# Performance work log

Hardware: AMD Instinct MI355X
Metric: run time of the kernel (lower is better)

Reference implementation:

```python
import jax, jax.numpy as jnp
import numpy as np
import math

B, N, D, H = 2, 2048, 512, 8
DH = D // H
HID = int(D * 16 / 3)  # 2730, SwiGLU hidden; chunks into 1365+1365
EPS = 1e-5


def _get_slopes(n):
    # n=8 is a power of two
    start = 2.0 ** (-2.0 ** (-(math.log2(n) - 3)))
    return np.array([start * (start ** i) for i in range(n)], dtype=np.float32)

_SLOPES = jnp.asarray(_get_slopes(H))  # [H]


def _ln(x, w, b):
    m = jnp.mean(x, axis=-1, keepdims=True)
    v = jnp.mean((x - m) ** 2, axis=-1, keepdims=True)
    return (x - m) * jax.lax.rsqrt(v + EPS) * w + b


def setup_inputs() -> dict:
    key = jax.random.key(0)
    ks = jax.random.split(key, 20)
    p = lambda k, s: jax.random.normal(k, s, jnp.float32) * 0.02
    return {
        "x": jax.random.normal(ks[0], (B, N, D), jnp.float32),
        "coords": jax.random.uniform(ks[1], (B, N, 2), jnp.float32) * 100.0,
        "q_w": p(ks[2], (D, D)), "q_b": jnp.zeros((D,), jnp.float32),
        "k_w": p(ks[3], (D, D)), "k_b": jnp.zeros((D,), jnp.float32),
        "v_w": p(ks[4], (D, D)), "v_b": jnp.zeros((D,), jnp.float32),
        "o_w": p(ks[5], (D, D)), "o_b": jnp.zeros((D,), jnp.float32),
        "gamma1": jnp.ones((D,), jnp.float32),
        "ln1_w": jnp.ones((D,), jnp.float32), "ln1_b": jnp.zeros((D,), jnp.float32),
        "fc1_w": p(ks[6], (HID, D)), "fc1_b": jnp.zeros((HID,), jnp.float32),
        "fc2_w": p(ks[7], (D, HID // 2)), "fc2_b": jnp.zeros((D,), jnp.float32),
        "gamma2": jnp.ones((D,), jnp.float32),
        "ln2_w": jnp.ones((D,), jnp.float32), "ln2_b": jnp.zeros((D,), jnp.float32),
    }


def reference(x, coords, q_w, q_b, k_w, k_b, v_w, v_b, o_w, o_b, gamma1,
              ln1_w, ln1_b, fc1_w, fc1_b, fc2_w, fc2_b, gamma2, ln2_w, ln2_b):
    # ---- residual1: distance-ALiBi attention (eval mode: x + gamma1*attn(norm(x)))
    xn = _ln(x, ln1_w, ln1_b)
    q = (xn @ q_w.T + q_b).reshape(B, N, H, DH).transpose(0, 2, 1, 3)  # [b,h,n,dh]
    k = (xn @ k_w.T + k_b).reshape(B, N, H, DH).transpose(0, 2, 1, 3)
    v = (xn @ v_w.T + v_b).reshape(B, N, H, DH).transpose(0, 2, 1, 3)
    # pairwise Euclidean distance of tile coords -> [b,n,n]
    diff = coords[:, :, None, :] - coords[:, None, :, :]
    dist = jnp.sqrt(jnp.sum(diff * diff, axis=-1))
    attn_bias = -_SLOPES[None, :, None, None] * dist[:, None, :, :]  # [b,h,n,n]
    scale = 1.0 / math.sqrt(DH)
    scores = jnp.einsum('bhqd,bhkd->bhqk', q, k) * scale + attn_bias
    attn = jax.nn.softmax(scores, axis=-1)
    ctx = jnp.einsum('bhqk,bhkd->bhqd', attn, v)
    ctx = ctx.transpose(0, 2, 1, 3).reshape(B, N, D)
    attn_out = ctx @ o_w.T + o_b
    x = x + gamma1 * attn_out
    # ---- residual2: SwiGLU-style MLP (eval mode: x + gamma2*mlp(norm(x)))
    xn2 = _ln(x, ln2_w, ln2_b)
    hpre = xn2 @ fc1_w.T + fc1_b  # [b,n,HID]
    h1, h2 = jnp.split(hpre, 2, axis=-1)
    mlp_out = (jax.nn.silu(h1) * h2) @ fc2_w.T + fc2_b
    return x + gamma2 * mlp_out
```

## Files before the change

### kernel.cpp

```cpp
#include <hip/hip_runtime.h>
#include <math.h>

#define Bdim  2
#define Nseq  2048
#define Dmod  512
#define Hn    8
#define DHd   64
#define HID   2730
#define HHALF 1365
#define HC    1408
#define NPACK 2816
#define ROWS  4096
#define NSPLIT 2
#define KT_PER (Nseq / 64 / NSPLIT)

typedef __bf16 bf16x8 __attribute__((ext_vector_type(8)));
typedef __bf16 bf16x4 __attribute__((ext_vector_type(4)));
typedef float  f32x4  __attribute__((ext_vector_type(4)));

__device__ __forceinline__ void glds16(const __bf16* g, __bf16* l) {
    __builtin_amdgcn_global_load_lds(
        (const __attribute__((address_space(1))) void*)g,
        (__attribute__((address_space(3))) void*)l, 16, 0, 0);
}

__device__ __forceinline__ void ln_body(
    int row, int tid, const float* __restrict__ x, const float* __restrict__ w,
    const float* __restrict__ b, __bf16* __restrict__ out)
{
    const float* xr = x + (size_t)row * Dmod;
    float2 v = *(const float2*)(xr + tid * 2);
    float s  = v.x + v.y;
    float sq = v.x * v.x + v.y * v.y;
#pragma unroll
    for (int m = 1; m < 64; m <<= 1) {
        s  += __shfl_xor(s, m, 64);
        sq += __shfl_xor(sq, m, 64);
    }
    __shared__ float ss[4], ssq[4];
    const int wv = tid >> 6;
    if ((tid & 63) == 0) { ss[wv] = s; ssq[wv] = sq; }
    __syncthreads();
    s  = ss[0] + ss[1] + ss[2] + ss[3];
    sq = ssq[0] + ssq[1] + ssq[2] + ssq[3];
    const float mean = s * (1.0f / Dmod);
    const float var  = sq * (1.0f / Dmod) - mean * mean;
    const float rstd = rsqrtf(var + 1e-5f);
    float2 wv2 = *(const float2*)(w + tid * 2);
    float2 bv2 = *(const float2*)(b + tid * 2);
    __bf16* orow = out + (size_t)row * Dmod + tid * 2;
    orow[0] = (__bf16)((v.x - mean) * rstd * wv2.x + bv2.x);
    orow[1] = (__bf16)((v.y - mean) * rstd * wv2.y + bv2.y);
}

#define SEG0 (1536*512)
#define SEG1 (512*512)
#define SEG2 (NPACK*512)
#define SEG3 (512*HC)
#define CONV_BLOCKS ((SEG0 + SEG1 + SEG2 + SEG3) / 256)
__global__ __launch_bounds__(256) void convert_ln(
    const float* __restrict__ q_w, const float* __restrict__ k_w,
    const float* __restrict__ v_w, const float* __restrict__ o_w,
    const float* __restrict__ fc1_w, const float* __restrict__ fc2_w,
    __bf16* __restrict__ wqkv, __bf16* __restrict__ wo,
    __bf16* __restrict__ wfc1p, __bf16* __restrict__ wfc2p,
    const float* __restrict__ x, const float* __restrict__ ln1w,
    const float* __restrict__ ln1b, __bf16* __restrict__ xn)
{
    if (blockIdx.x >= CONV_BLOCKS) {
        ln_body(blockIdx.x - CONV_BLOCKS, threadIdx.x, x, ln1w, ln1b, xn);
        return;
    }
    int idx = blockIdx.x * 256 + threadIdx.x;
    if (idx < SEG0) {
        int n = idx >> 9, k = idx & 511;
        float v = (n < 512) ? q_w[n * 512 + k]
                : (n < 1024) ? k_w[(n - 512) * 512 + k]
                : v_w[(n - 1024) * 512 + k];
        wqkv[idx] = (__bf16)v;
        return;
    }
    idx -= SEG0;
    if (idx < SEG1) { wo[idx] = (__bf16)o_w[idx]; return; }
    idx -= SEG1;
    if (idx < SEG2) {
        int n = idx >> 9, k = idx & 511;
        int j = n >> 5, u = n & 31;
        int base = j * 16 + (u & 15);
        float v = 0.0f;
        if (base < HHALF) {
            int hidx = base + ((u & 16) ? HHALF : 0);
            v = fc1_w[(size_t)hidx * 512 + k];
        }
        wfc1p[idx] = (__bf16)v;
        return;
    }
    idx -= SEG2;
    if (idx < SEG3) {
        int n = idx / HC, k = idx - n * HC;
        float v = (k < HHALF) ? fc2_w[(size_t)n * HHALF + k] : 0.0f;
        wfc2p[idx] = (__bf16)v;
    }
}

__global__ __launch_bounds__(256) void ln_kernel(
    const float* __restrict__ x, const float* __restrict__ w,
    const float* __restrict__ b, __bf16* __restrict__ out)
{
    ln_body(blockIdx.x, threadIdx.x, x, w, b, out);
}

__global__ __launch_bounds__(512) void gemm_res(
    const __bf16* __restrict__ A, int lda,
    const __bf16* __restrict__ Bw, int ldb,
    const float* __restrict__ bias, int K,
    float* __restrict__ out_f32, int ld_out,
    const float* __restrict__ res, const float* __restrict__ g)
{
    __shared__ __bf16 smem[2 * 64 * 64];
    __bf16* As = smem;
    __bf16* Bs = smem + 64 * 64;
    const int tid  = threadIdx.x;
    const int wave = tid >> 6, lane = tid & 63;
    const int t    = lane & 15, quad = lane >> 4;
    const int kg   = wave >> 2, wv = wave & 3;
    const int m0   = blockIdx.x * 64;
    const int n0   = blockIdx.y * 64;

    const int srow = tid >> 3;
    const int gch  = ((tid & 7) ^ (srow & 7)) * 8;
    const __bf16* aptr = A  + (size_t)(m0 + srow) * lda + gch;
    const __bf16* bptr = Bw + (size_t)(n0 + srow) * ldb + gch;

    const int arow = wv * 16 + t;
    const int aoff = arow * 64 + (((kg * 4 + quad) ^ (arow & 7)) * 8);
    int boffs[4];
#pragma unroll
    for (int ct = 0; ct < 4; ++ct) {
        int brow = ct * 16 + t;
        boffs[ct] = brow * 64 + (((kg * 4 + quad) ^ (brow & 7)) * 8);
    }

    f32x4 acc[4] = {};
    for (int k0 = 0; k0 < K; k0 += 64) {
        __syncthreads();
        glds16(aptr + k0, As + tid * 8);
        glds16(bptr + k0, Bs + tid * 8);
        __syncthreads();
        bf16x8 a = *(const bf16x8*)(As + aoff);
#pragma unroll
        for (int ct = 0; ct < 4; ++ct) {
            bf16x8 b = *(const bf16x8*)(Bs + boffs[ct]);
            acc[ct] = __builtin_amdgcn_mfma_f32_16x16x32_bf16(a, b, acc[ct], 0, 0, 0);
        }
    }

    __syncthreads();
    if (kg == 1) {
        float* dst = (float*)smem + ((size_t)wv * 64 + lane) * 16;
#pragma unroll
        for (int ct = 0; ct < 4; ++ct) *(f32x4*)(dst + ct * 4) = acc[ct];
    }
    __syncthreads();
    if (kg == 0) {
        const float* src = (const float*)smem + ((size_t)wv * 64 + lane) * 16;
        const int row_base = m0 + wv * 16 + quad * 4;
#pragma unroll
        for (int ct = 0; ct < 4; ++ct) {
            f32x4 other = *(const f32x4*)(src + ct * 4);
            const int col = n0 + ct * 16 + t;
            const float bb = bias[col];
#pragma unroll
            for (int r = 0; r < 4; ++r) {
                const int row = row_base + r;
                out_f32[(size_t)row * ld_out + col] =
                    res[(size_t)row * ld_out + col] +
                    g[col] * (acc[ct][r] + other[r] + bb);
            }
        }
    }
}

#define LDT 136
__global__ __launch_bounds__(256) void qkv_gemm128(
    const __bf16* __restrict__ A, const __bf16* __restrict__ W,
    const float* __restrict__ qb_, const float* __restrict__ kb_,
    const float* __restrict__ vb_,
    __bf16* __restrict__ qk, __bf16* __restrict__ vtg)
{
    __shared__ __bf16 smem[64 * LDT];
    __bf16* As = smem;
    __bf16* Bs = smem + 4096;
    const int tid  = threadIdx.x;
    const int wave = tid >> 6, lane = tid & 63;
    const int t    = lane & 15, quad = lane >> 4;
    const int m0   = blockIdx.x * 128, n0 = blockIdx.y * 128;
    const int mr   = (wave & 1) * 64,  nr = (wave >> 1) * 64;
    const int ra0 = tid >> 2,          ca0 = (tid & 3) * 8;
    const int ra1 = (tid + 256) >> 2,  ca1 = (tid & 3) * 8;

    f32x4 acc[4][4] = {};

    for (int k0 = 0; k0 < Dmod; k0 += 32) {
        __syncthreads();
        glds16(A + (size_t)(m0 + ra0) * Dmod + k0 + ca0, As + tid * 8);
        glds16(A + (size_t)(m0 + ra1) * Dmod + k0 + ca1, As + (tid + 256) * 8);
        glds16(W + (size_t)(n0 + ra0) * Dmod + k0 + ca0, Bs + tid * 8);
        glds16(W + (size_t)(n0 + ra1) * Dmod + k0 + ca1, Bs + (tid + 256) * 8);
        __syncthreads();
        bf16x8 af[4], bfr[4];
#pragma unroll
        for (int mi = 0; mi < 4; ++mi)
            af[mi] = *(const bf16x8*)(As + (mr + mi * 16 + t) * 32 + quad * 8);
#pragma unroll
        for (int ni = 0; ni < 4; ++ni)
            bfr[ni] = *(const bf16x8*)(Bs + (nr + ni * 16 + t) * 32 + quad * 8);
#pragma unroll
        for (int mi = 0; mi < 4; ++mi)
#pragma unroll
            for (int ni = 0; ni < 4; ++ni)
                acc[mi][ni] = __builtin_amdgcn_mfma_f32_16x16x32_bf16(af[mi], bfr[ni], acc[mi][ni], 0, 0, 0);
    }

    const int y = blockIdx.y;
    if (y < 8) {
#pragma unroll
        for (int mi = 0; mi < 4; ++mi) {
            const int row_base = m0 + mr + mi * 16 + quad * 4;
#pragma unroll
            for (int ni = 0; ni < 4; ++ni) {
                const int col = n0 + nr + ni * 16 + t;
                const float bb = (col < 512) ? qb_[col] : kb_[col - 512];
#pragma unroll
                for (int r = 0; r < 4; ++r)
                    qk[(size_t)(row_base + r) * 1024 + col] = (__bf16)(acc[mi][ni][r] + bb);
            }
        }
    } else {
        const int tok0 = m0 & 2047;
        const int bI   = m0 >> 11;
#pragma unroll
        for (int half = 0; half < 2; ++half) {
            __syncthreads();
            if ((wave >> 1) == half) {
#pragma unroll
                for (int ni = 0; ni < 4; ++ni) {
                    const int dh = ni * 16 + t;
                    const float bb = vb_[(y - 8) * 128 + half * 64 + dh];
#pragma unroll
                    for (int mi = 0; mi < 4; ++mi) {
                        const int n = mr + mi * 16 + quad * 4;
                        bf16x4 pk;
#pragma unroll
                        for (int r = 0; r < 4; ++r) pk[r] = (__bf16)(acc[mi][ni][r] + bb);
                        *(bf16x4*)(smem + dh * LDT + n) = pk;
                    }
                }
            }
            __syncthreads();
            const int hh = (y - 8) * 2 + half;
            const size_t rowbase = (size_t)(bI * 8 + hh) * 64;
#pragma unroll
            for (int j = 0; j < 4; ++j) {
                int chunk = tid + j * 256;
                int dr = chunk >> 4, cc = (chunk & 15) * 8;
                bf16x8 vv = *(const bf16x8*)(smem + dr * LDT + cc);
                *(bf16x8*)(vtg + (rowbase + dr) * Nseq + tok0 + cc) = vv;
            }
        }
    }
}

__global__ __launch_bounds__(256) void fc1_gemm128(
    const __bf16* __restrict__ A, const __bf16* __restrict__ W,
    const float* __restrict__ fc1_b_, __bf16* __restrict__ out)
{
    __shared__ __bf16 As[128 * 32];
    __shared__ __bf16 Bs[128 * 32];
    const int tid  = threadIdx.x;
    const int wave = tid >> 6, lane = tid & 63;
    const int t    = lane & 15, quad = lane >> 4;
    const int m0   = blockIdx.x * 128, n0 = blockIdx.y * 128;
    const int mr   = (wave & 1) * 64,  nr = (wave >> 1) * 64;
    const int ra0 = tid >> 2,          ca0 = (tid & 3) * 8;
    const int ra1 = (tid + 256) >> 2,  ca1 = (tid & 3) * 8;

    f32x4 acc[4][4] = {};

    for (int k0 = 0; k0 < Dmod; k0 += 32) {
        __syncthreads();
        glds16(A + (size_t)(m0 + ra0) * Dmod + k0 + ca0, As + tid * 8);
        glds16(A + (size_t)(m0 + ra1) * Dmod + k0 + ca1, As + (tid + 256) * 8);
        glds16(W + (size_t)(n0 + ra0) * Dmod + k0 + ca0, Bs + tid * 8);
        glds16(W + (size_t)(n0 + ra1) * Dmod + k0 + ca1, Bs + (tid + 256) * 8);
        __syncthreads();
        bf16x8 af[4], bfr[4];
#pragma unroll
        for (int mi = 0; mi < 4; ++mi)
            af[mi] = *(const bf16x8*)(As + (mr + mi * 16 + t) * 32 + quad * 8);
#pragma unroll
        for (int ni = 0; ni < 4; ++ni)
            bfr[ni] = *(const bf16x8*)(Bs + (nr + ni * 16 + t) * 32 + quad * 8);
#pragma unroll
        for (int mi = 0; mi < 4; ++mi)
#pragma unroll
            for (int ni = 0; ni < 4; ++ni)
                acc[mi][ni] = __builtin_amdgcn_mfma_f32_16x16x32_bf16(af[mi], bfr[ni], acc[mi][ni], 0, 0, 0);
    }

#pragma unroll
    for (int mi = 0; mi < 4; ++mi) {
        const int row_base = m0 + mr + mi * 16 + quad * 4;
#pragma unroll
        for (int gI = 0; gI < 2; ++gI) {
            const int base = n0 + nr + gI * 32;
            const int hb = (base >> 5) * 16 + t;
            const bool valid = hb < HHALF;
            const float b1 = valid ? fc1_b_[hb] : 0.0f;
            const float b2 = valid ? fc1_b_[HHALF + hb] : 0.0f;
#pragma unroll
            for (int r = 0; r < 4; ++r) {
                float a = acc[mi][2 * gI][r] + b1;
                float c = acc[mi][2 * gI + 1][r] + b2;
                float sw = a / (1.0f + __expf(-a)) * c;
                out[(size_t)(row_base + r) * HC + hb] = (__bf16)sw;
            }
        }
    }
}

__global__ __launch_bounds__(256) void attn_kernel(
    const __bf16* __restrict__ qk, const __bf16* __restrict__ vt,
    const float* __restrict__ coords,
    __bf16* __restrict__ op, float* __restrict__ lp)
{
    constexpr int LD = 72;
    __shared__ __bf16 Ks[64][LD];
    __shared__ __bf16 Vt[64][LD];
    __shared__ __bf16 Ps[64][LD];
    __shared__ float2 kco[64];

    const int qt = blockIdx.x, h = blockIdx.y;
    const int s = blockIdx.z >> 1, b = blockIdx.z & 1;
    const int bh = b * Hn + h;
    const int tid = threadIdx.x;
    const int wave = tid >> 6, lane = tid & 63;
    const int t = lane & 15, quad = lane >> 4;
    const float c1 = 0.125f * 1.44269504f;
    const float d1 = exp2f(-(float)(h + 1)) * 1.44269504f;
    const int kt0 = s * KT_PER, kt1 = kt0 + KT_PER;

    const int qrow = qt * 64 + wave * 16 + t;
    const size_t qbase = (size_t)(b * Nseq + qrow) * 1024 + h * DHd;
    bf16x8 bq0 = *(const bf16x8*)(qk + qbase + quad * 8);
    bf16x8 bq1 = *(const bf16x8*)(qk + qbase + 32 + quad * 8);
    float2 qc = *(const float2*)(coords + (size_t)(b * Nseq + qrow) * 2);
    const float qx = qc.x, qy = qc.y;

    const int sr = tid >> 3, scc = (tid & 7) * 8;
    const __bf16* kbase = qk + (size_t)(b * Nseq) * 1024 + 512 + h * DHd;
    const __bf16* vbase = vt + (size_t)(bh * 64) * Nseq;

    bf16x8 kreg0, kreg1, vreg0, vreg1;
    float2 kcreg = {0.f, 0.f};
    {
        const int kn0 = kt0 * 64;
        kreg0 = *(const bf16x8*)(kbase + (size_t)(kn0 + sr) * 1024 + scc);
        kreg1 = *(const bf16x8*)(kbase + (size_t)(kn0 + sr + 32) * 1024 + scc);
        vreg0 = *(const bf16x8*)(vbase + (size_t)sr * Nseq + kn0 + scc);
        vreg1 = *(const bf16x8*)(vbase + (size_t)(sr + 32) * Nseq + kn0 + scc);
        if (tid < 64) kcreg = *(const float2*)(coords + (size_t)(b * Nseq + kn0 + tid) * 2);
    }

    f32x4 o[4] = {};
    float lrun = 0.0f;

    for (int kt = kt0; kt < kt1; ++kt) {
        __syncthreads();
        *(bf16x8*)(&Ks[sr][scc])      = kreg0;
        *(bf16x8*)(&Ks[sr + 32][scc]) = kreg1;
        *(bf16x8*)(&Vt[sr][scc])      = vreg0;
        *(bf16x8*)(&Vt[sr + 32][scc]) = vreg1;
        if (tid < 64) kco[tid] = kcreg;
        __syncthreads();
        if (kt + 1 < kt1) {
            const int kn = (kt + 1) * 64;
            kreg0 = *(const bf16x8*)(kbase + (size_t)(kn + sr) * 1024 + scc);
            kreg1 = *(const bf16x8*)(kbase + (size_t)(kn + sr + 32) * 1024 + scc);
            vreg0 = *(const bf16x8*)(vbase + (size_t)sr * Nseq + kn + scc);
            vreg1 = *(const bf16x8*)(vbase + (size_t)(sr + 32) * Nseq + kn + scc);
            if (tid < 64) kcreg = *(const float2*)(coords + (size_t)(b * Nseq + kn + tid) * 2);
        }

        f32x4 sA[4];
#pragma unroll
        for (int am = 0; am < 4; ++am) {
            bf16x8 a0 = *(const bf16x8*)(&Ks[am * 16 + t][quad * 8]);
            bf16x8 a1 = *(const bf16x8*)(&Ks[am * 16 + t][32 + quad * 8]);
            f32x4 z = {};
            z = __builtin_amdgcn_mfma_f32_16x16x32_bf16(a0, bq0, z, 0, 0, 0);
            sA[am] = __builtin_amdgcn_mfma_f32_16x16x32_bf16(a1, bq1, z, 0, 0, 0);
        }

        float p[4][4];
#pragma unroll
        for (int am = 0; am < 4; ++am)
#pragma unroll
            for (int r = 0; r < 4; ++r) {
                float2 kc = kco[am * 16 + quad * 4 + r];
                float dx = qx - kc.x, dy = qy - kc.y;
                float dist = __builtin_amdgcn_sqrtf(dx * dx + dy * dy);
                float e = __builtin_amdgcn_exp2f(sA[am][r] * c1 - d1 * dist);
                p[am][r] = e;
                lrun += e;
            }

#pragma unroll
        for (int am = 0; am < 4; ++am) {
            bf16x4 pk;
#pragma unroll
            for (int r = 0; r < 4; ++r) pk[r] = (__bf16)p[am][r];
            *(bf16x4*)(&Ps[wave * 16 + t][am * 16 + quad * 4]) = pk;
        }

        bf16x8 ap0 = *(const bf16x8*)(&Ps[wave * 16 + t][quad * 8]);
        bf16x8 ap1 = *(const bf16x8*)(&Ps[wave * 16 + t][32 + quad * 8]);
#pragma unroll
        for (int ct = 0; ct < 4; ++ct) {
            bf16x8 bv0 = *(const bf16x8*)(&Vt[ct * 16 + t][quad * 8]);
            bf16x8 bv1 = *(const bf16x8*)(&Vt[ct * 16 + t][32 + quad * 8]);
            o[ct] = __builtin_amdgcn_mfma_f32_16x16x32_bf16(ap0, bv0, o[ct], 0, 0, 0);
            o[ct] = __builtin_amdgcn_mfma_f32_16x16x32_bf16(ap1, bv1, o[ct], 0, 0, 0);
        }
    }

    lrun += __shfl_xor(lrun, 16, 64);
    lrun += __shfl_xor(lrun, 32, 64);
    if (quad == 0)
        lp[(((size_t)s * Bdim + b) * Hn + h) * Nseq + qt * 64 + wave * 16 + t] = lrun;

    const int orow_base = qt * 64 + wave * 16 + quad * 4;
#pragma unroll
    for (int ct = 0; ct < 4; ++ct)
#pragma unroll
        for (int r = 0; r < 4; ++r) {
            size_t row = (size_t)s * ROWS + b * Nseq + orow_base + r;
            op[row * Dmod + h * DHd + ct * 16 + t] = (__bf16)o[ct][r];
        }
}

__global__ __launch_bounds__(256) void merge_kernel(
    const __bf16* __restrict__ op, const float* __restrict__ lp,
    __bf16* __restrict__ ctx)
{
    int idx = blockIdx.x * 256 + threadIdx.x;
    int row = idx >> 7, c4 = (idx & 127) * 4;
    int h = c4 >> 6;
    int b = row >> 11, n = row & 2047;
    float l = 0.0f;
#pragma unroll
    for (int s = 0; s < NSPLIT; ++s)
        l += lp[(((size_t)s * Bdim + b) * Hn + h) * Nseq + n];
    float rl = __builtin_amdgcn_rcpf(l);
    float oa[4] = {0.f, 0.f, 0.f, 0.f};
#pragma unroll
    for (int s = 0; s < NSPLIT; ++s) {
        bf16x4 ov = *(const bf16x4*)(op + ((size_t)s * ROWS + row) * Dmod + c4);
#pragma unroll
        for (int j = 0; j < 4; ++j) oa[j] += (float)ov[j];
    }
    bf16x4 r;
#pragma unroll
    for (int j = 0; j < 4; ++j) r[j] = (__bf16)(oa[j] * rl);
    *(bf16x4*)(ctx + (size_t)row * Dmod + c4) = r;
}

extern "C" void kernel_launch(void* const* d_in, const int* in_sizes, int n_in,
                              void* d_out, int out_size, void* d_ws, size_t ws_size,
                              hipStream_t stream)
{
    (void)in_sizes; (void)n_in; (void)out_size; (void)ws_size;
    const float* x      = (const float*)d_in[0];
    const float* coords = (const float*)d_in[1];
    const float* q_w    = (const float*)d_in[2];
    const float* q_b    = (const float*)d_in[3];
    const float* k_w    = (const float*)d_in[4];
    const float* k_b    = (const float*)d_in[5];
    const float* v_w    = (const float*)d_in[6];
    const float* v_b    = (const float*)d_in[7];
    const float* o_w    = (const float*)d_in[8];
    const float* o_b    = (const float*)d_in[9];
    const float* gamma1 = (const float*)d_in[10];
    const float* ln1_w  = (const float*)d_in[11];
    const float* ln1_b  = (const float*)d_in[12];
    const float* fc1_w  = (const float*)d_in[13];
    const float* fc1_b  = (const float*)d_in[14];
    const float* fc2_w  = (const float*)d_in[15];
    const float* fc2_b  = (const float*)d_in[16];
    const float* gamma2 = (const float*)d_in[17];
    const float* ln2_w  = (const float*)d_in[18];
    const float* ln2_b  = (const float*)d_in[19];

    size_t off = 0;
    auto alloc = [&](size_t bytes) {
        void* p = (char*)d_ws + off;
        off += (bytes + 255) & ~(size_t)255;
        return p;
    };
    __bf16* wqkv  = (__bf16*)alloc((size_t)1536 * 512 * 2);
    __bf16* wo    = (__bf16*)alloc((size_t)512 * 512 * 2);
    __bf16* wfc1p = (__bf16*)alloc((size_t)NPACK * 512 * 2);
    __bf16* wfc2p = (__bf16*)alloc((size_t)512 * HC * 2);
    __bf16* xn    = (__bf16*)alloc((size_t)ROWS * Dmod * 2);
    __bf16* xn2   = (__bf16*)alloc((size_t)ROWS * Dmod * 2);
    __bf16* qkb   = (__bf16*)alloc((size_t)ROWS * 1024 * 2);
    __bf16* vtg   = (__bf16*)alloc((size_t)Bdim * Hn * DHd * Nseq * 2);
    __bf16* ctxb  = (__bf16*)alloc((size_t)ROWS * Dmod * 2);
    float*  x1    = (float*)alloc((size_t)ROWS * Dmod * 4);
    __bf16* hcomb = (__bf16*)alloc((size_t)ROWS * HC * 2);
    __bf16* opb   = (__bf16*)alloc((size_t)NSPLIT * ROWS * Dmod * 2);
    float*  lpb   = (float*)alloc((size_t)NSPLIT * Bdim * Hn * Nseq * 4);

    convert_ln<<<CONV_BLOCKS + ROWS, 256, 0, stream>>>(
        q_w, k_w, v_w, o_w, fc1_w, fc2_w, wqkv, wo, wfc1p, wfc2p,
        x, ln1_w, ln1_b, xn);

    qkv_gemm128<<<dim3(ROWS / 128, 12), 256, 0, stream>>>(xn, wqkv, q_b, k_b, v_b, qkb, vtg);

    attn_kernel<<<dim3(Nseq / 64, Hn, Bdim * NSPLIT), 256, 0, stream>>>(
        qkb, vtg, coords, opb, lpb);
    merge_kernel<<<(ROWS * 128 + 255) / 256, 256, 0, stream>>>(opb, lpb, ctxb);

    gemm_res<<<dim3(ROWS / 64, Dmod / 64), 512, 0, stream>>>(
        ctxb, Dmod, wo, Dmod, o_b, Dmod, x1, Dmod, x, gamma1);

    ln_kernel<<<ROWS, 256, 0, stream>>>(x1, ln2_w, ln2_b, xn2);

    fc1_gemm128<<<dim3(ROWS / 128, NPACK / 128), 256, 0, stream>>>(xn2, wfc1p, fc1_b, hcomb);

    gemm_res<<<dim3(ROWS / 64, Dmod / 64), 512, 0, stream>>>(
        hcomb, HC, wfc2p, HC, fc2_b, HC, (float*)d_out, Dmod, x1, gamma2);
}
```

Before: 218.4 us.

## Fuse split-attention merge into out-proj GEMM and store residual x1 as bf16

Removes the separate merge kernel: the out-projection GEMM now loads both partial attention outputs, sums them, and normalizes by the combined softmax denominator while staging its A tile. The intermediate residual x1 is stored in bf16 instead of fp32, which halves its traffic through LN2 and the final residual add. This drops one launch and one round trip of the context tensor. In exchange, the A-tile loads become synchronous register loads instead of async global-to-LDS, and the residual stream loses precision.

Result: faster. 213.5 us (-2.3%).

```diff
diff --git a/kernel.cpp b/kernel.cpp
--- a/kernel.cpp
+++ b/kernel.cpp
@@ -12,10 +12,10 @@
 #define NPACK 2816
 #define ROWS  4096
 #define NSPLIT 2
-#define KT_PER (Nseq / 64 / NSPLIT)
 
 typedef __bf16 bf16x8 __attribute__((ext_vector_type(8)));
 typedef __bf16 bf16x4 __attribute__((ext_vector_type(4)));
+typedef __bf16 bf16x2 __attribute__((ext_vector_type(2)));
 typedef float  f32x4  __attribute__((ext_vector_type(4)));
 
 __device__ __forceinline__ void glds16(const __bf16* g, __bf16* l) {
@@ -24,14 +24,12 @@
         (__attribute__((address_space(3))) void*)l, 16, 0, 0);
 }
 
-__device__ __forceinline__ void ln_body(
-    int row, int tid, const float* __restrict__ x, const float* __restrict__ w,
-    const float* __restrict__ b, __bf16* __restrict__ out)
-{
-    const float* xr = x + (size_t)row * Dmod;
-    float2 v = *(const float2*)(xr + tid * 2);
-    float s  = v.x + v.y;
-    float sq = v.x * v.x + v.y * v.y;
+__device__ __forceinline__ void ln_core(
+    int tid, float vx, float vy, const float* __restrict__ w,
+    const float* __restrict__ b, __bf16* __restrict__ orow)
+{
+    float s  = vx + vy;
+    float sq = vx * vx + vy * vy;
 #pragma unroll
     for (int m = 1; m < 64; m <<= 1) {
         s  += __shfl_xor(s, m, 64);
@@ -48,9 +46,8 @@
     const float rstd = rsqrtf(var + 1e-5f);
     float2 wv2 = *(const float2*)(w + tid * 2);
     float2 bv2 = *(const float2*)(b + tid * 2);
-    __bf16* orow = out + (size_t)row * Dmod + tid * 2;
-    orow[0] = (__bf16)((v.x - mean) * rstd * wv2.x + bv2.x);
-    orow[1] = (__bf16)((v.y - mean) * rstd * wv2.y + bv2.y);
+    orow[0] = (__bf16)((vx - mean) * rstd * wv2.x + bv2.x);
+    orow[1] = (__bf16)((vy - mean) * rstd * wv2.y + bv2.y);
 }
 
 #define SEG0 (1536*512)
@@ -68,7 +65,9 @@
     const float* __restrict__ ln1b, __bf16* __restrict__ xn)
 {
     if (blockIdx.x >= CONV_BLOCKS) {
-        ln_body(blockIdx.x - CONV_BLOCKS, threadIdx.x, x, ln1w, ln1b, xn);
+        const int row = blockIdx.x - CONV_BLOCKS, tid = threadIdx.x;
+        float2 v = *(const float2*)(x + (size_t)row * Dmod + tid * 2);
+        ln_core(tid, v.x, v.y, ln1w, ln1b, xn + (size_t)row * Dmod + tid * 2);
         return;
     }
     int idx = blockIdx.x * 256 + threadIdx.x;
@@ -103,19 +102,23 @@
     }
 }
 
-__global__ __launch_bounds__(256) void ln_kernel(
-    const float* __restrict__ x, const float* __restrict__ w,
+__global__ __launch_bounds__(256) void ln_kernel_bf16(
+    const __bf16* __restrict__ x, const float* __restrict__ w,
     const float* __restrict__ b, __bf16* __restrict__ out)
 {
-    ln_body(blockIdx.x, threadIdx.x, x, w, b, out);
-}
-
+    const int row = blockIdx.x, tid = threadIdx.x;
+    bf16x2 v2 = *(const bf16x2*)(x + (size_t)row * Dmod + tid * 2);
+    ln_core(tid, (float)v2[0], (float)v2[1], w, b, out + (size_t)row * Dmod + tid * 2);
+}
+
+template<int MODE>
 __global__ __launch_bounds__(512) void gemm_res(
     const __bf16* __restrict__ A, int lda,
+    const __bf16* __restrict__ opA, const float* __restrict__ lpA,
     const __bf16* __restrict__ Bw, int ldb,
     const float* __restrict__ bias, int K,
-    float* __restrict__ out_f32, int ld_out,
-    const float* __restrict__ res, const float* __restrict__ g)
+    void* __restrict__ outp, const void* __restrict__ resp,
+    const float* __restrict__ g)
 {
     __shared__ __bf16 smem[2 * 64 * 64];
     __bf16* As = smem;
@@ -129,7 +132,9 @@
 
     const int srow = tid >> 3;
     const int gch  = ((tid & 7) ^ (srow & 7)) * 8;
-    const __bf16* aptr = A  + (size_t)(m0 + srow) * lda + gch;
+    const int grow = m0 + srow;
+    const int bI   = grow >> 11, nn = grow & 2047;
+    const __bf16* aptr = A  + (size_t)grow * lda + gch;
     const __bf16* bptr = Bw + (size_t)(n0 + srow) * ldb + gch;
 
     const int arow = wv * 16 + t;
@@ -144,7 +149,22 @@
     f32x4 acc[4] = {};
     for (int k0 = 0; k0 < K; k0 += 64) {
         __syncthreads();
-        glds16(aptr + k0, As + tid * 8);
+        if (MODE == 0) {
+            const int kk = k0 + gch;
+            const int h = kk >> 6;
+            float l = lpA[((size_t)(bI * Hn) + h) * Nseq + nn]
+                    + lpA[((size_t)((Bdim + bI) * Hn) + h) * Nseq + nn];
+            float rl = __builtin_amdgcn_rcpf(l);
+            bf16x8 a0 = *(const bf16x8*)(opA + (size_t)grow * Dmod + kk);
+            bf16x8 a1 = *(const bf16x8*)(opA + ((size_t)ROWS + grow) * Dmod + kk);
+            bf16x8 mg;
+#pragma unroll
+            for (int j = 0; j < 8; ++j)
+                mg[j] = (__bf16)(((float)a0[j] + (float)a1[j]) * rl);
+            *(bf16x8*)(As + tid * 8) = mg;
+        } else {
+            glds16(aptr + k0, As + tid * 8);
+        }
         glds16(bptr + k0, Bs + tid * 8);
         __syncthreads();
         bf16x8 a = *(const bf16x8*)(As + aoff);
@@ -173,9 +193,14 @@
 #pragma unroll
             for (int r = 0; r < 4; ++r) {
                 const int row = row_base + r;
-                out_f32[(size_t)row * ld_out + col] =
-                    res[(size_t)row * ld_out + col] +
-                    g[col] * (acc[ct][r] + other[r] + bb);
+                const float v = (acc[ct][r] + other[r] + bb) * g[col];
+                if (MODE == 0) {
+                    float rv = ((const float*)resp)[(size_t)row * Dmod + col];
+                    ((__bf16*)outp)[(size_t)row * Dmod + col] = (__bf16)(rv + v);
+                } else {
+                    float rv = (float)((const __bf16*)resp)[(size_t)row * Dmod + col];
+                    ((float*)outp)[(size_t)row * Dmod + col] = rv + v;
+                }
             }
         }
     }
@@ -332,7 +357,7 @@
 __global__ __launch_bounds__(256) void attn_kernel(
     const __bf16* __restrict__ qk, const __bf16* __restrict__ vt,
     const float* __restrict__ coords,
-    __bf16* __restrict__ op, float* __restrict__ lp)
+    __bf16* __restrict__ op, float* __restrict__ lp, int ktper)
 {
     constexpr int LD = 72;
     __shared__ __bf16 Ks[64][LD];
@@ -348,7 +373,6 @@
     const int t = lane & 15, quad = lane >> 4;
     const float c1 = 0.125f * 1.44269504f;
     const float d1 = exp2f(-(float)(h + 1)) * 1.44269504f;
-    const int kt0 = s * KT_PER, kt1 = kt0 + KT_PER;
 
     const int qrow = qt * 64 + wave * 16 + t;
     const size_t qbase = (size_t)(b * Nseq + qrow) * 1024 + h * DHd;
@@ -363,19 +387,17 @@
 
     bf16x8 kreg0, kreg1, vreg0, vreg1;
     float2 kcreg = {0.f, 0.f};
-    {
-        const int kn0 = kt0 * 64;
-        kreg0 = *(const bf16x8*)(kbase + (size_t)(kn0 + sr) * 1024 + scc);
-        kreg1 = *(const bf16x8*)(kbase + (size_t)(kn0 + sr + 32) * 1024 + scc);
-        vreg0 = *(const bf16x8*)(vbase + (size_t)sr * Nseq + kn0 + scc);
-        vreg1 = *(const bf16x8*)(vbase + (size_t)(sr + 32) * Nseq + kn0 + scc);
-        if (tid < 64) kcreg = *(const float2*)(coords + (size_t)(b * Nseq + kn0 + tid) * 2);
-    }
+    int kn = s * ktper * 64;
+    kreg0 = *(const bf16x8*)(kbase + (size_t)(kn + sr) * 1024 + scc);
+    kreg1 = *(const bf16x8*)(kbase + (size_t)(kn + sr + 32) * 1024 + scc);
+    vreg0 = *(const bf16x8*)(vbase + (size_t)sr * Nseq + kn + scc);
+    vreg1 = *(const bf16x8*)(vbase + (size_t)(sr + 32) * Nseq + kn + scc);
+    if (tid < 64) kcreg = *(const float2*)(coords + (size_t)(b * Nseq + kn + tid) * 2);
 
     f32x4 o[4] = {};
     float lrun = 0.0f;
 
-    for (int kt = kt0; kt < kt1; ++kt) {
+    for (int it = 0; it < ktper; ++it) {
         __syncthreads();
         *(bf16x8*)(&Ks[sr][scc])      = kreg0;
         *(bf16x8*)(&Ks[sr + 32][scc]) = kreg1;
@@ -383,13 +405,13 @@
         *(bf16x8*)(&Vt[sr + 32][scc]) = vreg1;
         if (tid < 64) kco[tid] = kcreg;
         __syncthreads();
-        if (kt + 1 < kt1) {
-            const int kn = (kt + 1) * 64;
-            kreg0 = *(const bf16x8*)(kbase + (size_t)(kn + sr) * 1024 + scc);
-            kreg1 = *(const bf16x8*)(kbase + (size_t)(kn + sr + 32) * 1024 + scc);
-            vreg0 = *(const bf16x8*)(vbase + (size_t)sr * Nseq + kn + scc);
-            vreg1 = *(const bf16x8*)(vbase + (size_t)(sr + 32) * Nseq + kn + scc);
-            if (tid < 64) kcreg = *(const float2*)(coords + (size_t)(b * Nseq + kn + tid) * 2);
+        if (it + 1 < ktper) {
+            const int k2 = kn + 64;
+            kreg0 = *(const bf16x8*)(kbase + (size_t)(k2 + sr) * 1024 + scc);
+            kreg1 = *(const bf16x8*)(kbase + (size_t)(k2 + sr + 32) * 1024 + scc);
+            vreg0 = *(const bf16x8*)(vbase + (size_t)sr * Nseq + k2 + scc);
+            vreg1 = *(const bf16x8*)(vbase + (size_t)(sr + 32) * Nseq + k2 + scc);
+            if (tid < 64) kcreg = *(const float2*)(coords + (size_t)(b * Nseq + k2 + tid) * 2);
         }
 
         f32x4 sA[4];
@@ -432,6 +454,7 @@
             o[ct] = __builtin_amdgcn_mfma_f32_16x16x32_bf16(ap0, bv0, o[ct], 0, 0, 0);
             o[ct] = __builtin_amdgcn_mfma_f32_16x16x32_bf16(ap1, bv1, o[ct], 0, 0, 0);
         }
+        kn += 64;
     }
 
     lrun += __shfl_xor(lrun, 16, 64);
@@ -447,32 +470,6 @@
             size_t row = (size_t)s * ROWS + b * Nseq + orow_base + r;
             op[row * Dmod + h * DHd + ct * 16 + t] = (__bf16)o[ct][r];
         }
-}
-
-__global__ __launch_bounds__(256) void merge_kernel(
-    const __bf16* __restrict__ op, const float* __restrict__ lp,
-    __bf16* __restrict__ ctx)
-{
-    int idx = blockIdx.x * 256 + threadIdx.x;
-    int row = idx >> 7, c4 = (idx & 127) * 4;
-    int h = c4 >> 6;
-    int b = row >> 11, n = row & 2047;
-    float l = 0.0f;
-#pragma unroll
-    for (int s = 0; s < NSPLIT; ++s)
-        l += lp[(((size_t)s * Bdim + b) * Hn + h) * Nseq + n];
-    float rl = __builtin_amdgcn_rcpf(l);
-    float oa[4] = {0.f, 0.f, 0.f, 0.f};
-#pragma unroll
-    for (int s = 0; s < NSPLIT; ++s) {
-        bf16x4 ov = *(const bf16x4*)(op + ((size_t)s * ROWS + row) * Dmod + c4);
-#pragma unroll
-        for (int j = 0; j < 4; ++j) oa[j] += (float)ov[j];
-    }
-    bf16x4 r;
-#pragma unroll
-    for (int j = 0; j < 4; ++j) r[j] = (__bf16)(oa[j] * rl);
-    *(bf16x4*)(ctx + (size_t)row * Dmod + c4) = r;
 }
 
 extern "C" void kernel_launch(void* const* d_in, const int* in_sizes, int n_in,
@@ -515,8 +512,7 @@
     __bf16* xn2   = (__bf16*)alloc((size_t)ROWS * Dmod * 2);
     __bf16* qkb   = (__bf16*)alloc((size_t)ROWS * 1024 * 2);
     __bf16* vtg   = (__bf16*)alloc((size_t)Bdim * Hn * DHd * Nseq * 2);
-    __bf16* ctxb  = (__bf16*)alloc((size_t)ROWS * Dmod * 2);
-    float*  x1    = (float*)alloc((size_t)ROWS * Dmod * 4);
+    __bf16* x1    = (__bf16*)alloc((size_t)ROWS * Dmod * 2);
     __bf16* hcomb = (__bf16*)alloc((size_t)ROWS * HC * 2);
     __bf16* opb   = (__bf16*)alloc((size_t)NSPLIT * ROWS * Dmod * 2);
     float*  lpb   = (float*)alloc((size_t)NSPLIT * Bdim * Hn * Nseq * 4);
@@ -528,16 +524,15 @@
     qkv_gemm128<<<dim3(ROWS / 128, 12), 256, 0, stream>>>(xn, wqkv, q_b, k_b, v_b, qkb, vtg);
 
     attn_kernel<<<dim3(Nseq / 64, Hn, Bdim * NSPLIT), 256, 0, stream>>>(
-        qkb, vtg, coords, opb, lpb);
-    merge_kernel<<<(ROWS * 128 + 255) / 256, 256, 0, stream>>>(opb, lpb, ctxb);
-
-    gemm_res<<<dim3(ROWS / 64, Dmod / 64), 512, 0, stream>>>(
-        ctxb, Dmod, wo, Dmod, o_b, Dmod, x1, Dmod, x, gamma1);
-
-    ln_kernel<<<ROWS, 256, 0, stream>>>(x1, ln2_w, ln2_b, xn2);
+        qkb, vtg, coords, opb, lpb, Nseq / 64 / NSPLIT);
+
+    gemm_res<0><<<dim3(ROWS / 64, Dmod / 64), 512, 0, stream>>>(
+        nullptr, Dmod, opb, lpb, wo, Dmod, o_b, Dmod, (void*)x1, (const void*)x, gamma1);
+
+    ln_kernel_bf16<<<ROWS, 256, 0, stream>>>(x1, ln2_w, ln2_b, xn2);
 
     fc1_gemm128<<<dim3(ROWS / 128, NPACK / 128), 256, 0, stream>>>(xn2, wfc1p, fc1_b, hcomb);
 
-    gemm_res<<<dim3(ROWS / 64, Dmod / 64), 512, 0, stream>>>(
-        hcomb, HC, wfc2p, HC, fc2_b, HC, (float*)d_out, Dmod, x1, gamma2);
-}
+    gemm_res<1><<<dim3(ROWS / 64, Dmod / 64), 512, 0, stream>>>(
+        hcomb, HC, nullptr, nullptr, wfc2p, HC, fc2_b, HC, d_out, (const void*)x1, gamma2);
+}
```
